# Kernel tuning notes

Measured on AMD Instinct MI355X. Metric: run time of the kernel, lower is better.

## Reference

```python
import jax, jax.numpy as jnp
import numpy as np

N = 100000      # nodes
D = 128         # embed_dim == hidden_size (code forces them equal)
M = 3           # edge_types / meta-paths
L = 2           # layers
E = 1600000     # edges per meta-path (avg degree 16)
ATT = 128       # semantic attention hidden size


def setup_inputs():
    key = jax.random.key(0)
    ks = jax.random.split(key, 8)
    x = jnp.arange(N)
    edge_index0 = jax.random.randint(ks[0], (2, E), 0, N)
    edge_index1 = jax.random.randint(ks[1], (2, E), 0, N)
    edge_index2 = jax.random.randint(ks[2], (2, E), 0, N)
    embed_table = jax.random.normal(ks[3], (N, D), dtype=jnp.float32) * 0.02
    W = jax.random.normal(ks[4], (L, M, D, D), dtype=jnp.float32) / np.sqrt(D)
    B = jnp.zeros((L, M, D), dtype=jnp.float32)
    att_w1 = jax.random.normal(ks[5], (L, D, ATT), dtype=jnp.float32) / np.sqrt(D)
    att_b1 = jnp.zeros((L, ATT), dtype=jnp.float32)
    att_w2 = jax.random.normal(ks[6], (L, ATT, 1), dtype=jnp.float32) / np.sqrt(ATT)
    return dict(x=x, edge_index0=edge_index0, edge_index1=edge_index1,
                edge_index2=edge_index2, embed_table=embed_table, W=W, B=B,
                att_w1=att_w1, att_b1=att_b1, att_w2=att_w2)


def _gcn_conv(h, W, b, src, dst):
    # GCNConv(normalize=True): self-loops already appended to src/dst.
    deg = jax.ops.segment_sum(jnp.ones_like(dst, dtype=h.dtype), dst, num_segments=N)
    dinv = jnp.where(deg > 0, jax.lax.rsqrt(deg), 0.0)
    norm = dinv[src] * dinv[dst]                       # [E+N]
    hw = h @ W                                         # [N, D]
    msg = hw[src] * norm[:, None]                      # gather + scale
    return jax.ops.segment_sum(msg, dst, num_segments=N) + b


def reference(x, edge_index0, edge_index1, edge_index2,
              embed_table, W, B, att_w1, att_b1, att_w2):
    edges = [edge_index0, edge_index1, edge_index2]
    loops = jnp.arange(N)
    srcs = [jnp.concatenate([e[0], loops]) for e in edges]
    dsts = [jnp.concatenate([e[1], loops]) for e in edges]

    h = embed_table[x]                                 # [N, D]
    for l in range(L):
        sems = [_gcn_conv(h, W[l, m], B[l, m], srcs[m], dsts[m]) for m in range(M)]
        z = jnp.stack(sems, axis=1)                    # [N, M, D]
        # semantic attention: Linear -> tanh -> Linear(no bias), softmax over M
        w = jnp.tanh(z @ att_w1[l] + att_b1[l]) @ att_w2[l]   # [N, M, 1]
        beta = jax.nn.softmax(w, axis=1)
        h = (beta * z).sum(axis=1)                     # [N, D]
    return jax.nn.log_softmax(h, axis=1)
```

## Files before the change

kernel.cpp:

```cpp
#include <hip/hip_runtime.h>
#include <hip/hip_bf16.h>

#define NN 100000
#define DD 128
#define MM 3
#define EE 1600000
#define CH_NODES 512
#define NC ((NN + CH_NODES - 1) / CH_NODES)
#define ECAP 10752
#define ECHTOT ((size_t)NC * ECAP)
#define TILE_E 8192
#define NTILES ((EE + TILE_E - 1) / TILE_E)
#define HSCALE 64.0f
#define HINV (1.0f / 64.0f)
#define PADMARK 0xFFFFFFFFu

typedef unsigned int uint32_hip;
typedef short short8 __attribute__((ext_vector_type(8)));
typedef float floatx4 __attribute__((ext_vector_type(4)));
typedef float floatx2 __attribute__((ext_vector_type(2)));

__device__ __forceinline__ float bf2f(short s) {
  return __uint_as_float(((uint32_hip)(unsigned short)s) << 16);
}
__device__ __forceinline__ unsigned short f2bf(float f) {
  union { __hip_bfloat16 b; unsigned short u; } cv;
  cv.b = __float2bfloat16(f);
  return cv.u;
}
__device__ __forceinline__ uint32_hip packbf2(float x, float y) {
  return (uint32_hip)f2bf(x) | ((uint32_hip)f2bf(y) << 16);
}
__device__ __forceinline__ float tanh_apx(float x) {
  float e = __expf(2.0f * x);
  return 1.0f - 2.0f / (e + 1.0f);
}
__device__ __forceinline__ uint32_hip pack_fp8x4(float a, float b, float c, float d) {
  uint32_hip w = 0;
  w = __builtin_amdgcn_cvt_pk_fp8_f32(a, b, w, false);
  w = __builtin_amdgcn_cvt_pk_fp8_f32(c, d, w, true);
  return w;
}
__device__ __forceinline__ float h2f(uint32_hip u) {
  union { unsigned short us; _Float16 h; } cv;
  cv.us = (unsigned short)u;
  return (float)cv.h;
}
__device__ __forceinline__ unsigned short f2h(float f) {
  union { unsigned short us; _Float16 h; } cv;
  cv.h = (_Float16)f;
  return cv.us;
}
__device__ __forceinline__ void dec16(uint4 hv, floatx2* f) {
  f[0] = __builtin_amdgcn_cvt_pk_f32_fp8((int)hv.x, false);
  f[1] = __builtin_amdgcn_cvt_pk_f32_fp8((int)hv.x, true);
  f[2] = __builtin_amdgcn_cvt_pk_f32_fp8((int)hv.y, false);
  f[3] = __builtin_amdgcn_cvt_pk_f32_fp8((int)hv.y, true);
  f[4] = __builtin_amdgcn_cvt_pk_f32_fp8((int)hv.z, false);
  f[5] = __builtin_amdgcn_cvt_pk_f32_fp8((int)hv.z, true);
  f[6] = __builtin_amdgcn_cvt_pk_f32_fp8((int)hv.w, false);
  f[7] = __builtin_amdgcn_cvt_pk_f32_fp8((int)hv.w, true);
}

__global__ __launch_bounds__(256) void hist1_kernel(const int* __restrict__ e0,
                                                    const int* __restrict__ e1,
                                                    const int* __restrict__ e2,
                                                    int* __restrict__ thist) {
  __shared__ int hist[NC];
  int m = blockIdx.y, tile = blockIdx.x, t = threadIdx.x;
  const int* ei = (m == 0) ? e0 : (m == 1) ? e1 : e2;
  const int* dst = ei + EE;
  int beg = tile * TILE_E, end = min(beg + TILE_E, EE);
  if (t < NC) hist[t] = 0;
  __syncthreads();
  for (int e = beg + t; e < end; e += 256) atomicAdd(&hist[dst[e] >> 9], 1);
  __syncthreads();
  int* th = thist + (size_t)m * NC * NTILES + tile;
  if (t < NC) th[(size_t)t * NTILES] = hist[t];
}

__global__ __launch_bounds__(256) void scan1_kernel(int* __restrict__ thist,
                                                    int* __restrict__ ccount) {
  __shared__ int sw[256];
  int c = blockIdx.x, m = blockIdx.y, t = threadIdx.x;
  int* th = thist + ((size_t)m * NC + c) * NTILES;
  int v = (t < NTILES) ? th[t] : 0;
  sw[t] = v;
  __syncthreads();
  for (int off = 1; off < 256; off <<= 1) {
    int u = (t >= off) ? sw[t - off] : 0;
    __syncthreads();
    sw[t] += u;
    __syncthreads();
  }
  if (t < NTILES) th[t] = c * ECAP + sw[t] - v;
  if (t == NTILES - 1) ccount[m * NC + c] = sw[t];
}

__global__ __launch_bounds__(256) void scatter1_kernel(const int* __restrict__ e0,
                                                       const int* __restrict__ e1,
                                                       const int* __restrict__ e2,
                                                       const int* __restrict__ thist,
                                                       const int* __restrict__ ccount,
                                                       uint32_hip* __restrict__ lvl1) {
  __shared__ int gbase[NC];
  __shared__ int spos[NC];
  __shared__ int cur[NC];
  __shared__ int sw[256];
  __shared__ uint32_hip sval[TILE_E];
  __shared__ unsigned char sbuk[TILE_E];
  int m = blockIdx.y, tile = blockIdx.x, t = threadIdx.x;
  const int* ei = (m == 0) ? e0 : (m == 1) ? e1 : e2;
  const int* dst = ei + EE;
  const int* th = thist + (size_t)m * NC * NTILES + tile;
  int cnt = 0;
  if (t < NC) {
    int gb = th[(size_t)t * NTILES];
    int gn = (tile + 1 < NTILES) ? th[(size_t)t * NTILES + 1] : t * ECAP + ccount[m * NC + t];
    gbase[t] = gb;
    cnt = gn - gb;
  }
  sw[t] = cnt;
  __syncthreads();
  for (int off = 1; off < 256; off <<= 1) {
    int u = (t >= off) ? sw[t - off] : 0;
    __syncthreads();
    sw[t] += u;
    __syncthreads();
  }
  if (t < NC) {
    spos[t] = sw[t] - cnt;
    cur[t] = sw[t] - cnt;
  }
  __syncthreads();
  int beg = tile * TILE_E, end = min(beg + TILE_E, EE);
  int ct = end - beg;
  for (int e = beg + t; e < end; e += 256) {
    int s = ei[e], d = dst[e];
    int b = d >> 9;
    int r = atomicAdd(&cur[b], 1);
    sval[r] = (uint32_hip)s | ((uint32_hip)(d & 511) << 17);
    sbuk[r] = (unsigned char)b;
  }
  __syncthreads();
  uint32_hip* eb = lvl1 + (size_t)m * ECHTOT;
  for (int i = t; i < ct; i += 256) {
    int b = sbuk[i];
    eb[gbase[b] + (i - spos[b])] = sval[i];
  }
}

__global__ __launch_bounds__(256) void sort2_kernel(uint32_hip* __restrict__ lvl1,
                                                    const int* __restrict__ ccount,
                                                    int* __restrict__ astart,
                                                    unsigned short* __restrict__ sdeg,
                                                    int* __restrict__ cpad) {
  __shared__ uint32_hip ebl[ECAP];
  __shared__ int cnt[CH_NODES];
  __shared__ int pos[CH_NODES];
  __shared__ int sw[256];
  int m = blockIdx.y, c = blockIdx.x, t = threadIdx.x;
  int base = c * ECAP;
  int ct = ccount[m * NC + c];
  uint32_hip* eb = lvl1 + (size_t)m * ECHTOT + base;
  for (int e = t; e < ct; e += 256) ebl[e] = eb[e];
  cnt[t] = 0;
  cnt[t + 256] = 0;
  __syncthreads();
  for (int e = t; e < ct; e += 256) atomicAdd(&cnt[ebl[e] >> 17], 1);
  __syncthreads();
  int c0 = cnt[2 * t], c1 = cnt[2 * t + 1];
  int p0 = (c0 + 3) & ~3, p1 = (c1 + 3) & ~3;
  int s = p0 + p1;
  sw[t] = s;
  __syncthreads();
  for (int off = 1; off < 256; off <<= 1) {
    int u = (t >= off) ? sw[t - off] : 0;
    __syncthreads();
    sw[t] += u;
    __syncthreads();
  }
  int excl = sw[t] - s;
  pos[2 * t] = excl;
  pos[2 * t + 1] = excl + p0;
  int node0 = c * CH_NODES;
  {
    int n0 = node0 + 2 * t;
    if (n0 < NN) {
      astart[(size_t)m * NN + n0] = base + excl;
      sdeg[(size_t)m * NN + n0] = (unsigned short)c0;
    }
    int n1 = node0 + 2 * t + 1;
    if (n1 < NN) {
      astart[(size_t)m * NN + n1] = base + excl + p0;
      sdeg[(size_t)m * NN + n1] = (unsigned short)c1;
    }
  }
  if (t == 255) cpad[m * NC + c] = sw[255];
  __syncthreads();
  for (int e = t; e < ct; e += 256) {
    uint32_hip p = ebl[e];
    int q = atomicAdd(&pos[p >> 17], 1);
    eb[q] = p & 0x1FFFFu;
  }
  for (int i = c0; i < p0; ++i) eb[excl + i] = PADMARK;
  for (int i = c1; i < p1; ++i) eb[excl + p0 + i] = PADMARK;
}

__global__ void norm_embed_kernel(uint32_hip* __restrict__ lvl1, const int* __restrict__ cpad,
                                  const unsigned short* __restrict__ sdeg) {
  int m = blockIdx.y, c = blockIdx.x, t = threadIdx.x;
  int base = c * ECAP;
  int ct = cpad[m * NC + c];
  uint32_hip* eb = lvl1 + (size_t)m * ECHTOT + base;
  const unsigned short* sd = sdeg + (size_t)m * NN;
  for (int e = t; e < ct; e += 256) {
    uint32_hip p = eb[e];
    uint32_hip s = p & 0x1FFFFu;
    uint32_hip sc_ = (s < NN) ? s : 0;
    float dv = rsqrtf((float)(sd[sc_] + 1));
    eb[e] = (p == PADMARK) ? 0u : (s | ((uint32_hip)f2h(dv) << 17));
  }
}

__global__ __launch_bounds__(512) void degsort_kernel(const unsigned short* __restrict__ sdeg,
                                                      int* __restrict__ perm) {
  __shared__ int hist[512];
  __shared__ int pos[512];
  __shared__ int cur[512];
  int m = blockIdx.x, t = threadIdx.x;
  const unsigned short* sd = sdeg + (size_t)m * NN;
  hist[t] = 0;
  __syncthreads();
  for (int n = t; n < NN; n += 512) atomicAdd(&hist[min((int)sd[n], 511)], 1);
  __syncthreads();
  pos[t] = hist[t];
  __syncthreads();
  for (int off = 1; off < 512; off <<= 1) {
    int v = (t >= off) ? pos[t - off] : 0;
    __syncthreads();
    pos[t] += v;
    __syncthreads();
  }
  cur[t] = pos[t] - hist[t];
  __syncthreads();
  int* pm = perm + (size_t)m * NN;
  for (int n = t; n < NN; n += 512) {
    int d = min((int)sd[n], 511);
    int r = atomicAdd(&cur[d], 1);
    pm[r] = n;
  }
}

__global__ void embed_kernel(const int* __restrict__ x, const float* __restrict__ tbl,
                             uint32_hip* __restrict__ hq) {
  int i = blockIdx.x * 256 + threadIdx.x;
  if (i < NN * 32) {
    int n = i >> 5;
    int c = i & 31;
    float4 v = ((const float4*)tbl)[(size_t)x[n] * 32 + c];
    hq[(size_t)n * 32 + c] =
        pack_fp8x4(v.x * HSCALE, v.y * HSCALE, v.z * HSCALE, v.w * HSCALE);
  }
}

__global__ __launch_bounds__(256) void agg_kernel(const uint32_hip* __restrict__ hq,
                                                  const unsigned short* __restrict__ sdeg,
                                                  const int* __restrict__ astart,
                                                  const uint32_hip* __restrict__ csr,
                                                  const int* __restrict__ perm,
                                                  uint32_hip* __restrict__ zall) {
  int m = blockIdx.y;
  const unsigned short* sd = sdeg + (size_t)m * NN;
  const int* as_ = astart + (size_t)m * NN;
  const uint32_hip* cs = csr + (size_t)m * ECHTOT;
  const int* pm = perm + (size_t)m * NN;
  uint32_hip* zo = zall + (size_t)m * NN * 64;
  int t = threadIdx.x;
  int wave = t >> 6, lane = t & 63;
  int g = lane >> 3, l = lane & 7;
  int slot = blockIdx.x * 32 + wave * 8 + g;
  int n = pm[slot];
  int deg = sd[n];
  float di = rsqrtf((float)(deg + 1));
  floatx2 ac[8];
  {
    uint4 hv = *(const uint4*)(hq + (size_t)n * 32 + l * 4);
    floatx2 f[8];
    dec16(hv, f);
    floatx2 di2 = {di, di};
#pragma unroll
    for (int j = 0; j < 8; ++j) ac[j] = di2 * f[j];
  }
  int e = as_[n];
  int end = e + ((deg + 3) & ~3);
  while (__any(e < end)) {
    uint32_hip msk = (e < end) ? 0xFFFFFFFFu : 0u;
    uint4 ce = *(const uint4*)(cs + e);
    uint32_hip cearr[4] = {ce.x & msk, ce.y & msk, ce.z & msk, ce.w & msk};
#pragma unroll
    for (int k = 0; k < 4; ++k) {
      uint32_hip ck = cearr[k];
      float nk = h2f(ck >> 17);
      int sk = ck & 0x1FFFF;
      uint4 hk = *(const uint4*)(hq + (size_t)sk * 32 + l * 4);
      floatx2 fk[8];
      dec16(hk, fk);
      floatx2 n2 = {nk, nk};
#pragma unroll
      for (int j = 0; j < 8; ++j) ac[j] = __builtin_elementwise_fma(n2, fk[j], ac[j]);
    }
    e += 4;
  }
  float scv = di * HINV;
  floatx2 sc2 = {scv, scv};
#pragma unroll
  for (int j = 0; j < 8; ++j) ac[j] = ac[j] * sc2;
  uint4 w0, w1;
  w0.x = packbf2(ac[0].x, ac[0].y);
  w0.y = packbf2(ac[1].x, ac[1].y);
  w0.z = packbf2(ac[2].x, ac[2].y);
  w0.w = packbf2(ac[3].x, ac[3].y);
  w1.x = packbf2(ac[4].x, ac[4].y);
  w1.y = packbf2(ac[5].x, ac[5].y);
  w1.z = packbf2(ac[6].x, ac[6].y);
  w1.w = packbf2(ac[7].x, ac[7].y);
  uint32_hip* zr = zo + (size_t)n * 64 + l * 8;
  *(uint4*)zr = w0;
  *(uint4*)(zr + 4) = w1;
}

__global__ __launch_bounds__(256) void mfma_gemm_kernel(unsigned short* __restrict__ zall,
                                                        const float* __restrict__ Wall,
                                                        const float* __restrict__ Ball) {
  __shared__ unsigned short Wt[128 * 136];
  int m = blockIdx.y;
  const float* Wmat = Wall + (size_t)m * DD * DD;
  const float* bias = Ball + (size_t)m * DD;
  unsigned short* Z = zall + (size_t)m * NN * DD;
  int t = threadIdx.x;
  {
    uint32_hip* Wt_u = (uint32_hip*)Wt;
#pragma unroll
    for (int i = 0; i < 32; ++i) {
      int idx = i * 256 + t;
      int k2 = idx >> 7;
      int nn = idx & 127;
      float w0 = Wmat[(2 * k2) * 128 + nn];
      float w1 = Wmat[(2 * k2 + 1) * 128 + nn];
      Wt_u[nn * 68 + k2] = packbf2(w0, w1);
    }
  }
  __syncthreads();
  int wave = t >> 6, lane = t & 63;
  int quad = lane >> 4, ln = lane & 15;
  int rowbase = blockIdx.x * 64 + wave * 16;
  int arow = rowbase + ln;
  int arowc = (arow < NN) ? arow : (NN - 1);
  const short8* zrow = (const short8*)(Z + (size_t)arowc * 128);
  floatx4 acc[8];
#pragma unroll
  for (int c = 0; c < 8; ++c) acc[c] = (floatx4){0.f, 0.f, 0.f, 0.f};
#pragma unroll
  for (int kt = 0; kt < 4; ++kt) {
    short8 a = zrow[kt * 4 + quad];
#pragma unroll
    for (int c = 0; c < 8; ++c) {
      const short8* bp = (const short8*)(Wt + (c * 16 + ln) * 136 + kt * 32 + quad * 8);
      acc[c] = __builtin_amdgcn_mfma_f32_16x16x32_bf16(a, *bp, acc[c], 0, 0, 0);
    }
  }
#pragma unroll
  for (int c = 0; c < 8; ++c) {
    int col = c * 16 + ln;
    float bs = bias[col];
#pragma unroll
    for (int r = 0; r < 4; ++r) {
      int grow = rowbase + quad * 4 + r;
      if (grow < NN) Z[(size_t)grow * 128 + col] = f2bf(acc[c][r] + bs);
    }
  }
}

__global__ __launch_bounds__(256) void att_combine_kernel(
    const unsigned short* __restrict__ Z, const float* __restrict__ W1,
    const float* __restrict__ b1, const float* __restrict__ w2,
    uint32_hip* __restrict__ hq, float* __restrict__ fout, int last) {
  __shared__ unsigned short Wt[128 * 136];
  __shared__ float sc[4][3][16];
  int t = threadIdx.x;
  {
    uint32_hip* Wt_u = (uint32_hip*)Wt;
#pragma unroll
    for (int i = 0; i < 32; ++i) {
      int idx = i * 256 + t;
      int k2 = idx >> 7;
      int nn = idx & 127;
      float w0 = W1[(2 * k2) * 128 + nn];
      float w1 = W1[(2 * k2 + 1) * 128 + nn];
      Wt_u[nn * 68 + k2] = packbf2(w0, w1);
    }
  }
  __syncthreads();
  int wave = t >> 6, lane = t & 63;
  int quad = lane >> 4, ln = lane & 15;
  int nodebase = blockIdx.x * 64 + wave * 16;
  int frow = nodebase + ln;
  int frowc = (frow < NN) ? frow : (NN - 1);
  short8 af[3][4];
#pragma unroll
  for (int m = 0; m < 3; ++m) {
    const short8* zr = (const short8*)(Z + ((size_t)m * NN + frowc) * 128);
#pragma unroll
    for (int kt = 0; kt < 4; ++kt) af[m][kt] = zr[kt * 4 + quad];
  }
#pragma unroll
  for (int m = 0; m < 3; ++m) {
    floatx4 acc[8];
#pragma unroll
    for (int c = 0; c < 8; ++c) acc[c] = (floatx4){0.f, 0.f, 0.f, 0.f};
#pragma unroll
    for (int kt = 0; kt < 4; ++kt) {
#pragma unroll
      for (int c = 0; c < 8; ++c) {
        const short8* bp = (const short8*)(Wt + (c * 16 + ln) * 136 + kt * 32 + quad * 8);
        acc[c] = __builtin_amdgcn_mfma_f32_16x16x32_bf16(af[m][kt], *bp, acc[c], 0, 0, 0);
      }
    }
    float rows[4] = {0.f, 0.f, 0.f, 0.f};
#pragma unroll
    for (int c = 0; c < 8; ++c) {
      int col = c * 16 + ln;
      float bb = b1[col];
      float ww = w2[col];
#pragma unroll
      for (int r = 0; r < 4; ++r) rows[r] += tanh_apx(acc[c][r] + bb) * ww;
    }
#pragma unroll
    for (int off = 8; off > 0; off >>= 1) {
#pragma unroll
      for (int r = 0; r < 4; ++r) rows[r] += __shfl_down(rows[r], off);
    }
    if (ln == 0) {
#pragma unroll
      for (int r = 0; r < 4; ++r) sc[wave][m][quad * 4 + r] = rows[r];
    }
  }
  __syncthreads();
  float s0 = sc[wave][0][ln], s1 = sc[wave][1][ln], s2 = sc[wave][2][ln];
  float mx = fmaxf(s0, fmaxf(s1, s2));
  float e0 = __expf(s0 - mx), e1 = __expf(s1 - mx), e2 = __expf(s2 - mx);
  float inv = 1.0f / (e0 + e1 + e2);
  float bb0 = e0 * inv, bb1 = e1 * inv, bb2 = e2 * inv;
  float o[4][8];
#pragma unroll
  for (int kt = 0; kt < 4; ++kt) {
#pragma unroll
    for (int j = 0; j < 8; ++j) {
      o[kt][j] = bb0 * bf2f(af[0][kt][j]) + bb1 * bf2f(af[1][kt][j]) + bb2 * bf2f(af[2][kt][j]);
    }
  }
  if (!last) {
    if (frow < NN) {
#pragma unroll
      for (int kt = 0; kt < 4; ++kt) {
        uint2 v;
        v.x = pack_fp8x4(o[kt][0] * HSCALE, o[kt][1] * HSCALE, o[kt][2] * HSCALE,
                         o[kt][3] * HSCALE);
        v.y = pack_fp8x4(o[kt][4] * HSCALE, o[kt][5] * HSCALE, o[kt][6] * HSCALE,
                         o[kt][7] * HSCALE);
        *(uint2*)&hq[(size_t)frow * 32 + kt * 8 + quad * 2] = v;
      }
    }
  } else {
    float vmx = o[0][0];
#pragma unroll
    for (int kt = 0; kt < 4; ++kt)
#pragma unroll
      for (int j = 0; j < 8; ++j) vmx = fmaxf(vmx, o[kt][j]);
    vmx = fmaxf(vmx, __shfl_xor(vmx, 16));
    vmx = fmaxf(vmx, __shfl_xor(vmx, 32));
    float ss = 0.f;
#pragma unroll
    for (int kt = 0; kt < 4; ++kt)
#pragma unroll
      for (int j = 0; j < 8; ++j) ss += __expf(o[kt][j] - vmx);
    ss += __shfl_xor(ss, 16);
    ss += __shfl_xor(ss, 32);
    float lse = vmx + logf(ss);
    if (frow < NN) {
#pragma unroll
      for (int kt = 0; kt < 4; ++kt) {
        float4 a, b;
        a.x = o[kt][0] - lse; a.y = o[kt][1] - lse; a.z = o[kt][2] - lse; a.w = o[kt][3] - lse;
        b.x = o[kt][4] - lse; b.y = o[kt][5] - lse; b.z = o[kt][6] - lse; b.w = o[kt][7] - lse;
        float* dst = fout + (size_t)frow * 128 + kt * 32 + quad * 8;
        *(float4*)dst = a;
        *(float4*)(dst + 4) = b;
      }
    }
  }
}

extern "C" void kernel_launch(void* const* d_in, const int* in_sizes, int n_in,
                              void* d_out, int out_size, void* d_ws, size_t ws_size,
                              hipStream_t stream) {
  const int* x = (const int*)d_in[0];
  const int* e0 = (const int*)d_in[1];
  const int* e1 = (const int*)d_in[2];
  const int* e2 = (const int*)d_in[3];
  const float* embed = (const float*)d_in[4];
  const float* W = (const float*)d_in[5];
  const float* B = (const float*)d_in[6];
  const float* aw1 = (const float*)d_in[7];
  const float* ab1 = (const float*)d_in[8];
  const float* aw2 = (const float*)d_in[9];
  float* out = (float*)d_out;
  uint32_hip* hq = (uint32_hip*)d_out;

  char* ws = (char*)d_ws;
  size_t off = 0;
  auto alloc = [&](size_t bytes) {
    void* p = ws + off;
    off += (bytes + 255) & ~(size_t)255;
    return p;
  };
  unsigned short* z = (unsigned short*)alloc((size_t)MM * NN * DD * 2);
  uint32_hip* lvl1 = (uint32_hip*)alloc((size_t)MM * ECHTOT * 4 + 4096);
  int* astart = (int*)alloc((size_t)MM * NN * 4);
  unsigned short* sdeg = (unsigned short*)alloc((size_t)MM * NN * 2);
  int* ccount = (int*)alloc((size_t)MM * NC * 4);
  int* cpad = (int*)alloc((size_t)MM * NC * 4);
  int* perm = (int*)alloc((size_t)MM * NN * 4);
  int* thist = (int*)alloc((size_t)MM * NC * NTILES * 4);

  dim3 bs(256);
  hist1_kernel<<<dim3(NTILES, 3), bs, 0, stream>>>(e0, e1, e2, thist);
  scan1_kernel<<<dim3(NC, 3), bs, 0, stream>>>(thist, ccount);
  scatter1_kernel<<<dim3(NTILES, 3), bs, 0, stream>>>(e0, e1, e2, thist, ccount, lvl1);
  sort2_kernel<<<dim3(NC, 3), bs, 0, stream>>>(lvl1, ccount, astart, sdeg, cpad);
  norm_embed_kernel<<<dim3(NC, 3), bs, 0, stream>>>(lvl1, cpad, sdeg);
  degsort_kernel<<<dim3(3), dim3(512), 0, stream>>>(sdeg, perm);
  embed_kernel<<<dim3((NN * 32 + 255) / 256), bs, 0, stream>>>(x, embed, hq);

  for (int l = 0; l < 2; ++l) {
    agg_kernel<<<dim3(NN / 32, 3), bs, 0, stream>>>(
        (const uint32_hip*)hq, sdeg, astart, lvl1, perm, (uint32_hip*)z);
    mfma_gemm_kernel<<<dim3((NN + 63) / 64, 3), bs, 0, stream>>>(
        z, W + (size_t)l * 3 * DD * DD, B + (size_t)l * 3 * DD);
    att_combine_kernel<<<dim3((NN + 63) / 64), bs, 0, stream>>>(
        z, aw1 + (size_t)l * DD * DD, ab1 + (size_t)l * DD, aw2 + (size_t)l * DD, hq, out, l == 1);
  }
}
```

Measured before the change: 695.4 us.

## Parallelize degree sort and pack per-node info; prefetch CSR edges in aggregation

The single-block-per-meta-path degree sort is replaced by a multi-block tiled histogram, two scan passes and a scatter. The scatter writes a packed per-node record (edge start, node id, degree) in descending-degree order. The aggregation kernel reads that one record instead of three dependent lookups, and it prefetches the next group of four CSR entries while the current group is processed. Costs are three extra kernel launches, a larger permutation buffer, and one extra out-of-range CSR load at the end of each node's edge list.

```diff
diff --git a/kernel.cpp b/kernel.cpp
--- a/kernel.cpp
+++ b/kernel.cpp
@@ -11,6 +11,10 @@
 #define ECHTOT ((size_t)NC * ECAP)
 #define TILE_E 8192
 #define NTILES ((EE + TILE_E - 1) / TILE_E)
+#define DTILE 2048
+#define NT2 ((NN + DTILE - 1) / DTILE)
+#define NT2P 52
+#define DBINS 512
 #define HSCALE 64.0f
 #define HINV (1.0f / 64.0f)
 #define PADMARK 0xFFFFFFFFu
@@ -223,32 +227,78 @@
   }
 }
 
-__global__ __launch_bounds__(512) void degsort_kernel(const unsigned short* __restrict__ sdeg,
-                                                      int* __restrict__ perm) {
-  __shared__ int hist[512];
-  __shared__ int pos[512];
-  __shared__ int cur[512];
-  int m = blockIdx.x, t = threadIdx.x;
+__global__ __launch_bounds__(256) void dhist_kernel(const unsigned short* __restrict__ sdeg,
+                                                    int* __restrict__ dthist) {
+  __shared__ int hist[DBINS];
+  int m = blockIdx.y, tile = blockIdx.x, t = threadIdx.x;
   const unsigned short* sd = sdeg + (size_t)m * NN;
   hist[t] = 0;
-  __syncthreads();
-  for (int n = t; n < NN; n += 512) atomicAdd(&hist[min((int)sd[n], 511)], 1);
-  __syncthreads();
-  pos[t] = hist[t];
-  __syncthreads();
-  for (int off = 1; off < 512; off <<= 1) {
-    int v = (t >= off) ? pos[t - off] : 0;
-    __syncthreads();
-    pos[t] += v;
-    __syncthreads();
-  }
-  cur[t] = pos[t] - hist[t];
-  __syncthreads();
-  int* pm = perm + (size_t)m * NN;
-  for (int n = t; n < NN; n += 512) {
-    int d = min((int)sd[n], 511);
-    int r = atomicAdd(&cur[d], 1);
-    pm[r] = n;
+  hist[t + 256] = 0;
+  __syncthreads();
+  int beg = tile * DTILE, end = min(beg + DTILE, NN);
+  for (int n = beg + t; n < end; n += 256) atomicAdd(&hist[min((int)sd[n], DBINS - 1)], 1);
+  __syncthreads();
+  int* th = dthist + ((size_t)m * DBINS) * NT2P + tile;
+  th[(size_t)t * NT2P] = hist[t];
+  th[(size_t)(t + 256) * NT2P] = hist[t + 256];
+}
+
+__global__ __launch_bounds__(64) void dscan_kernel(int* __restrict__ dthist,
+                                                   int* __restrict__ bintot) {
+  __shared__ int sw[64];
+  int bin = blockIdx.x, m = blockIdx.y, t = threadIdx.x;
+  int* th = dthist + ((size_t)m * DBINS + bin) * NT2P;
+  int v = (t < NT2) ? th[t] : 0;
+  sw[t] = v;
+  __syncthreads();
+  for (int off = 1; off < 64; off <<= 1) {
+    int u = (t >= off) ? sw[t - off] : 0;
+    __syncthreads();
+    sw[t] += u;
+    __syncthreads();
+  }
+  if (t < NT2) th[t] = sw[t] - v;
+  if (t == 63) bintot[m * DBINS + bin] = sw[63];
+}
+
+__global__ __launch_bounds__(512) void dscan2_kernel(const int* __restrict__ bintot,
+                                                     int* __restrict__ binbase) {
+  __shared__ int sw[DBINS];
+  int m = blockIdx.x, t = threadIdx.x;
+  int v = bintot[m * DBINS + t];
+  sw[t] = v;
+  __syncthreads();
+  for (int off = 1; off < DBINS; off <<= 1) {
+    int u = (t >= off) ? sw[t - off] : 0;
+    __syncthreads();
+    sw[t] += u;
+    __syncthreads();
+  }
+  binbase[m * DBINS + t] = sw[t] - v;
+}
+
+__global__ __launch_bounds__(256) void dscatter_kernel(const unsigned short* __restrict__ sdeg,
+                                                       const int* __restrict__ astart,
+                                                       const int* __restrict__ dthist,
+                                                       const int* __restrict__ binbase,
+                                                       uint2* __restrict__ pinfo) {
+  __shared__ int cur[DBINS];
+  int m = blockIdx.y, tile = blockIdx.x, t = threadIdx.x;
+  const unsigned short* sd = sdeg + (size_t)m * NN;
+  const int* as_ = astart + (size_t)m * NN;
+  for (int b = t; b < DBINS; b += 256)
+    cur[b] = binbase[m * DBINS + b] + dthist[((size_t)m * DBINS + b) * NT2P + tile];
+  __syncthreads();
+  uint2* pi = pinfo + (size_t)m * NN;
+  int beg = tile * DTILE, end = min(beg + DTILE, NN);
+  for (int n = beg + t; n < end; n += 256) {
+    int d = sd[n];
+    int r = atomicAdd(&cur[min(d, DBINS - 1)], 1);
+    int slot = NN - 1 - r;
+    uint2 v;
+    v.x = (uint32_hip)as_[n];
+    v.y = (uint32_hip)n | ((uint32_hip)d << 17);
+    pi[slot] = v;
   }
 }
 
@@ -265,23 +315,21 @@
 }
 
 __global__ __launch_bounds__(256) void agg_kernel(const uint32_hip* __restrict__ hq,
-                                                  const unsigned short* __restrict__ sdeg,
-                                                  const int* __restrict__ astart,
+                                                  const uint2* __restrict__ pinfo,
                                                   const uint32_hip* __restrict__ csr,
-                                                  const int* __restrict__ perm,
                                                   uint32_hip* __restrict__ zall) {
   int m = blockIdx.y;
-  const unsigned short* sd = sdeg + (size_t)m * NN;
-  const int* as_ = astart + (size_t)m * NN;
+  const uint2* pi_ = pinfo + (size_t)m * NN;
   const uint32_hip* cs = csr + (size_t)m * ECHTOT;
-  const int* pm = perm + (size_t)m * NN;
   uint32_hip* zo = zall + (size_t)m * NN * 64;
   int t = threadIdx.x;
   int wave = t >> 6, lane = t & 63;
   int g = lane >> 3, l = lane & 7;
   int slot = blockIdx.x * 32 + wave * 8 + g;
-  int n = pm[slot];
-  int deg = sd[n];
+  uint2 pi = pi_[slot];
+  int e = (int)pi.x;
+  int n = (int)(pi.y & 0x1FFFFu);
+  int deg = (int)(pi.y >> 17);
   float di = rsqrtf((float)(deg + 1));
   floatx2 ac[8];
   {
@@ -292,11 +340,12 @@
 #pragma unroll
     for (int j = 0; j < 8; ++j) ac[j] = di2 * f[j];
   }
-  int e = as_[n];
   int end = e + ((deg + 3) & ~3);
+  uint4 ce = *(const uint4*)(cs + e);
   while (__any(e < end)) {
+    int en = e + 4;
+    uint4 cn = *(const uint4*)(cs + en);
     uint32_hip msk = (e < end) ? 0xFFFFFFFFu : 0u;
-    uint4 ce = *(const uint4*)(cs + e);
     uint32_hip cearr[4] = {ce.x & msk, ce.y & msk, ce.z & msk, ce.w & msk};
 #pragma unroll
     for (int k = 0; k < 4; ++k) {
@@ -310,7 +359,8 @@
 #pragma unroll
       for (int j = 0; j < 8; ++j) ac[j] = __builtin_elementwise_fma(n2, fk[j], ac[j]);
     }
-    e += 4;
+    ce = cn;
+    e = en;
   }
   float scv = di * HINV;
   floatx2 sc2 = {scv, scv};
@@ -531,8 +581,11 @@
   unsigned short* sdeg = (unsigned short*)alloc((size_t)MM * NN * 2);
   int* ccount = (int*)alloc((size_t)MM * NC * 4);
   int* cpad = (int*)alloc((size_t)MM * NC * 4);
-  int* perm = (int*)alloc((size_t)MM * NN * 4);
+  uint2* pinfo = (uint2*)alloc((size_t)MM * NN * 8);
   int* thist = (int*)alloc((size_t)MM * NC * NTILES * 4);
+  int* dthist = (int*)alloc((size_t)MM * DBINS * NT2P * 4);
+  int* bintot = (int*)alloc((size_t)MM * DBINS * 4);
+  int* binbase = (int*)alloc((size_t)MM * DBINS * 4);
 
   dim3 bs(256);
   hist1_kernel<<<dim3(NTILES, 3), bs, 0, stream>>>(e0, e1, e2, thist);
@@ -540,12 +593,15 @@
   scatter1_kernel<<<dim3(NTILES, 3), bs, 0, stream>>>(e0, e1, e2, thist, ccount, lvl1);
   sort2_kernel<<<dim3(NC, 3), bs, 0, stream>>>(lvl1, ccount, astart, sdeg, cpad);
   norm_embed_kernel<<<dim3(NC, 3), bs, 0, stream>>>(lvl1, cpad, sdeg);
-  degsort_kernel<<<dim3(3), dim3(512), 0, stream>>>(sdeg, perm);
+  dhist_kernel<<<dim3(NT2, 3), bs, 0, stream>>>(sdeg, dthist);
+  dscan_kernel<<<dim3(DBINS, 3), dim3(64), 0, stream>>>(dthist, bintot);
+  dscan2_kernel<<<dim3(3), dim3(DBINS), 0, stream>>>(bintot, binbase);
+  dscatter_kernel<<<dim3(NT2, 3), bs, 0, stream>>>(sdeg, astart, dthist, binbase, pinfo);
   embed_kernel<<<dim3((NN * 32 + 255) / 256), bs, 0, stream>>>(x, embed, hq);
 
   for (int l = 0; l < 2; ++l) {
     agg_kernel<<<dim3(NN / 32, 3), bs, 0, stream>>>(
-        (const uint32_hip*)hq, sdeg, astart, lvl1, perm, (uint32_hip*)z);
+        (const uint32_hip*)hq, pinfo, lvl1, (uint32_hip*)z);
     mfma_gemm_kernel<<<dim3((NN + 63) / 64, 3), bs, 0, stream>>>(
         z, W + (size_t)l * 3 * DD * DD, B + (size_t)l * 3 * DD);
     att_combine_kernel<<<dim3((NN + 63) / 64), bs, 0, stream>>>(
```

New measurement: 654.9 us. -5.8%, faster.
